# Kernel optimization log

Hardware: AMD Instinct MI355X
Metric: run time of the kernel (lower is better)

Reference implementation:

```python
import jax, jax.numpy as jnp
import numpy as np

B, N, C = 4, 2048, 768
H = 12
D = C // H  # head_dim = 64


def setup_inputs() -> dict:
    key = jax.random.key(0)
    k1, k2, k3, k4, k5 = jax.random.split(key, 5)
    s = 0.02
    return {
        "x": jax.random.normal(k1, (B, N, C), dtype=jnp.float32),
        "qkv_w": jax.random.normal(k2, (3 * C, C), dtype=jnp.float32) * s,
        "qkv_b": jax.random.normal(k3, (3 * C,), dtype=jnp.float32) * s,
        "proj_w": jax.random.normal(k4, (C, C), dtype=jnp.float32) * s,
        "proj_b": jax.random.normal(k5, (C,), dtype=jnp.float32) * s,
    }


def reference(x, qkv_w, qkv_b, proj_w, proj_b):
    b, n, c = x.shape
    # qkv projection (torch Linear: x @ W.T + b) -> [B,N,3,H,D] -> [3,B,H,N,D]
    qkv = (x @ qkv_w.T + qkv_b).reshape(b, n, 3, H, D).transpose(2, 0, 3, 1, 4)
    q, k, v = qkv[0], qkv[1], qkv[2]
    scale = D ** (-0.5)
    attn = jnp.einsum("bhqd,bhkd->bhqk", q, k) * scale
    attn = jax.nn.softmax(attn, axis=-1)
    # dropout is identity in eval mode
    out = jnp.einsum("bhqk,bhkd->bhqd", attn, v)  # [B,H,N,D]
    out = out.transpose(0, 2, 1, 3).reshape(b, n, c)
    return out @ proj_w.T + proj_b
```

## Files before the change

### kernel.cpp

```cpp
#include <hip/hip_runtime.h>
#include <hip/hip_bf16.h>
#include <stdint.h>

typedef __bf16 bf16_t;
typedef __bf16 bf16x8 __attribute__((ext_vector_type(8)));
typedef float f32x4 __attribute__((ext_vector_type(4)));
typedef unsigned int u32x4 __attribute__((ext_vector_type(4)));

#define NB 4
#define NH 12
#define ND 64
#define NN 2048
#define NC 768

__device__ __forceinline__ void async_copy16(const bf16_t* g, bf16_t* l) {
    __builtin_amdgcn_global_load_lds((__attribute__((address_space(1))) void*)(void*)g,
                                     (__attribute__((address_space(3))) void*)l, 16, 0, 0);
}

__device__ __forceinline__ unsigned pack_bf2(float a, float b) {
    union { bf16_t e[2]; unsigned u; } t;
    t.e[0] = (bf16_t)a;
    t.e[1] = (bf16_t)b;
    return t.u;
}

__global__ void cast_kernel(const float* __restrict__ src, bf16_t* __restrict__ dst, int n4) {
    int i = blockIdx.x * blockDim.x + threadIdx.x;
    if (i >= n4) return;
    float4 v = ((const float4*)src)[i];
    union { bf16_t e[4]; uint2 u; } t;
    t.e[0] = (bf16_t)v.x; t.e[1] = (bf16_t)v.y; t.e[2] = (bf16_t)v.z; t.e[3] = (bf16_t)v.w;
    ((uint2*)dst)[i] = t.u;
}

__device__ __forceinline__ int vperm(int s) {
    return (s & 32) | (((s >> 2) & 3) << 3) | (((s >> 4) & 1) << 2) | (s & 3);
}


template <bool ISV>
__launch_bounds__(256)
__global__ void qkv_gemm_kernel(const bf16_t* __restrict__ X, const bf16_t* __restrict__ W,
                                const float* __restrict__ bias,
                                bf16_t* __restrict__ Q, bf16_t* __restrict__ K, bf16_t* __restrict__ V,
                                int n0base)
{
    __shared__ __align__(16) bf16_t sA[128 * 64];
    __shared__ __align__(16) bf16_t sB[128 * 64];
    const int tid  = threadIdx.x;
    const int lane = tid & 63;
    const int w    = tid >> 6;
    const int wm   = w & 1, wn = w >> 1;
    const int m0   = blockIdx.x * 128;
    const int n0   = n0base + blockIdx.y * 128;
    const int lrow = lane & 15;
    const int quad = lane >> 4;
    const int arow = lane >> 3;
    const int gch  = (lane & 7) ^ arow;

    const int colbase = n0 + wn * 64;

    f32x4 zero = {0.f, 0.f, 0.f, 0.f};
    f32x4 acc[4][4];
#pragma unroll
    for (int i = 0; i < 4; ++i)
#pragma unroll
        for (int j = 0; j < 4; ++j) acc[i][j] = zero;

    for (int kt = 0; kt < NC; kt += 64) {
        __syncthreads();
        for (int c = w; c < 16; c += 4) {
            async_copy16(X + (size_t)(m0 + c * 8 + arow) * NC + kt + gch * 8, sA + c * 512);
            async_copy16(W + (size_t)(n0 + c * 8 + arow) * NC + kt + gch * 8, sB + c * 512);
        }
        __syncthreads();
#pragma unroll
        for (int hh = 0; hh < 2; ++hh) {
            bf16x8 xf[4], wf[4];
#pragma unroll
            for (int i = 0; i < 4; ++i) {
                int r = wm * 64 + i * 16 + lrow;
                xf[i] = *(const bf16x8*)(sA + r * 64 + (((hh * 4 + quad) ^ (r & 7)) * 8));
            }
#pragma unroll
            for (int j = 0; j < 4; ++j) {
                int r = wn * 64 + j * 16 + lrow;
                wf[j] = *(const bf16x8*)(sB + r * 64 + (((hh * 4 + quad) ^ (r & 7)) * 8));
            }
#pragma unroll
            for (int i = 0; i < 4; ++i)
#pragma unroll
                for (int j = 0; j < 4; ++j) {
                    if (ISV)
                        acc[i][j] = __builtin_amdgcn_mfma_f32_16x16x32_bf16(xf[i], wf[j], acc[i][j], 0, 0, 0);
                    else
                        acc[i][j] = __builtin_amdgcn_mfma_f32_16x16x32_bf16(wf[j], xf[i], acc[i][j], 0, 0, 0);
                }
        }
    }

    const float qscale = 0.125f * 1.44269504088896340736f;

    if (!ISV) {
        const int t3 = colbase / NC;
        const int h  = (colbase % NC) / ND;
        bf16_t* outb = t3 ? K : Q;
#pragma unroll
        for (int j = 0; j < 4; ++j) {
            const int dcol = j * 16 + quad * 4;
            const float4 bv4 = *(const float4*)(bias + colbase + dcol);
#pragma unroll
            for (int i = 0; i < 4; ++i) {
                const int tok = m0 + wm * 64 + i * 16 + lrow;
                const int bb = tok >> 11;
                const int nn = tok & 2047;
                union { bf16_t e[4]; uint2 u; } pk;
#pragma unroll
                for (int p = 0; p < 4; ++p) {
                    float val = acc[i][j][p] + (&bv4.x)[p];
                    if (t3 == 0) val *= qscale;
                    pk.e[p] = (bf16_t)val;
                }
                *(uint2*)(outb + ((size_t)(bb * NH + h) * NN + nn) * ND + dcol) = pk.u;
            }
        }
    } else {
        const int h = (colbase - 2 * NC) / ND;
#pragma unroll
        for (int j = 0; j < 4; ++j) {
            const int d  = j * 16 + lrow;
            const float bv = bias[colbase + d];
#pragma unroll
            for (int i = 0; i < 4; ++i) {
                const int tok0 = m0 + wm * 64 + i * 16 + quad * 4;
                const int bb = tok0 >> 11;
                const int nn = tok0 & 2047;
                union { bf16_t e[4]; uint2 u; } pk;
#pragma unroll
                for (int p = 0; p < 4; ++p) pk.e[p] = (bf16_t)(acc[i][j][p] + bv);
                const int pos = (nn & ~63) | vperm(nn & 63);
                *(uint2*)(V + ((size_t)(bb * NH + h) * ND + d) * NN + pos) = pk.u;
            }
        }
    }
}

__launch_bounds__(256, 4)
__global__ void attn_kernel(const bf16_t* __restrict__ Q, const bf16_t* __restrict__ K,
                            const bf16_t* __restrict__ Vt, bf16_t* __restrict__ O)
{
    __shared__ __align__(16) bf16_t sKV[4][64 * 64];
    bf16_t* sQ = sKV[0];
    const int tid  = threadIdx.x;
    const int lane = tid & 63;
    const int w    = tid >> 6;
    const int qt   = blockIdx.x;
    const int h    = blockIdx.y;
    const int b    = blockIdx.z;
    const int lrow = lane & 15;
    const int quad = lane >> 4;
    const int arow = lane >> 3;
    const int gch  = (lane & 7) ^ arow;
    const size_t head_off = (size_t)(b * NH + h) * NN * ND;
    const bf16_t* qh = Q  + head_off;
    const bf16_t* kh = K  + head_off;
    const bf16_t* vh = Vt + head_off;

#pragma unroll
    for (int c = 0; c < 4; ++c)
        async_copy16(qh + (size_t)(qt * 128 + (w * 4 + c) * 8 + arow) * ND + gch * 8,
                     sQ + (w * 4 + c) * 512);
    __syncthreads();

    bf16x8 qb[2][2];
#pragma unroll
    for (int qi = 0; qi < 2; ++qi)
#pragma unroll
        for (int hh = 0; hh < 2; ++hh) {
            int r = w * 32 + qi * 16 + lrow;
            qb[qi][hh] = *(const bf16x8*)(sQ + r * 64 + (((hh * 4 + quad) ^ (r & 7)) * 8));
        }

    int off[4][2];
#pragma unroll
    for (int blk = 0; blk < 4; ++blk) {
        int r = blk * 16 + lrow;
        off[blk][0] = r * 64 + ((quad ^ (r & 7)) * 8);
        off[blk][1] = r * 64 + (((4 + quad) ^ (r & 7)) * 8);
    }

    f32x4 zero = {0.f, 0.f, 0.f, 0.f};
    f32x4 o[2][4];
#pragma unroll
    for (int qi = 0; qi < 2; ++qi)
#pragma unroll
        for (int db = 0; db < 4; ++db) o[qi][db] = zero;
    float l_i[2] = {0.f, 0.f};

    const bf16_t* kp = kh + (size_t)(w * 16 + arow) * ND + gch * 8;
    const bf16_t* vp = vh + (size_t)(w * 16 + arow) * NN + gch * 8;

    for (int it = 0; it < NN / 128; ++it) {
        __syncthreads();
        async_copy16(kp,               sKV[0] + w * 1024);
        async_copy16(kp + 8 * ND,      sKV[0] + w * 1024 + 512);
        async_copy16(kp + 64 * ND,     sKV[1] + w * 1024);
        async_copy16(kp + 72 * ND,     sKV[1] + w * 1024 + 512);
        async_copy16(vp,               sKV[2] + w * 1024);
        async_copy16(vp + 8 * NN,      sKV[2] + w * 1024 + 512);
        async_copy16(vp + 64,          sKV[3] + w * 1024);
        async_copy16(vp + 8 * NN + 64, sKV[3] + w * 1024 + 512);
        __syncthreads();
        kp += 128 * ND;
        vp += 128;

#pragma unroll
        for (int half = 0; half < 2; ++half) {
            const bf16_t* sKh = sKV[half];
            const bf16_t* sVh = sKV[2 + half];

            f32x4 s[2][4];
#pragma unroll
            for (int blk = 0; blk < 4; ++blk) {
                bf16x8 a0 = *(const bf16x8*)(sKh + off[blk][0]);
                bf16x8 a1 = *(const bf16x8*)(sKh + off[blk][1]);
#pragma unroll
                for (int qi = 0; qi < 2; ++qi) {
                    f32x4 z = zero;
                    z = __builtin_amdgcn_mfma_f32_16x16x32_bf16(a0, qb[qi][0], z, 0, 0, 0);
                    z = __builtin_amdgcn_mfma_f32_16x16x32_bf16(a1, qb[qi][1], z, 0, 0, 0);
                    s[qi][blk] = z;
                }
            }

            bf16x8 pe[2][2];
#pragma unroll
            for (int qi = 0; qi < 2; ++qi) {
                u32x4 pu0 = {0, 0, 0, 0}, pu1 = {0, 0, 0, 0};
                float r0 = 0.f, r1 = 0.f;
#pragma unroll
                for (int blk = 0; blk < 4; ++blk) {
                    float e0 = __builtin_amdgcn_exp2f(s[qi][blk][0]);
                    float e1 = __builtin_amdgcn_exp2f(s[qi][blk][1]);
                    float e2 = __builtin_amdgcn_exp2f(s[qi][blk][2]);
                    float e3 = __builtin_amdgcn_exp2f(s[qi][blk][3]);
                    r0 += e0 + e1;
                    r1 += e2 + e3;
                    unsigned lo = pack_bf2(e0, e1), hi = pack_bf2(e2, e3);
                    if (blk == 0)      { pu0[0] = lo; pu0[1] = hi; }
                    else if (blk == 1) { pu0[2] = lo; pu0[3] = hi; }
                    else if (blk == 2) { pu1[0] = lo; pu1[1] = hi; }
                    else               { pu1[2] = lo; pu1[3] = hi; }
                }
                pe[qi][0] = __builtin_bit_cast(bf16x8, pu0);
                pe[qi][1] = __builtin_bit_cast(bf16x8, pu1);
                l_i[qi] += r0 + r1;
            }

#pragma unroll
            for (int db = 0; db < 4; ++db) {
                bf16x8 v0 = *(const bf16x8*)(sVh + off[db][0]);
                bf16x8 v1 = *(const bf16x8*)(sVh + off[db][1]);
#pragma unroll
                for (int qi = 0; qi < 2; ++qi) {
                    o[qi][db] = __builtin_amdgcn_mfma_f32_16x16x32_bf16(v0, pe[qi][0], o[qi][db], 0, 0, 0);
                    o[qi][db] = __builtin_amdgcn_mfma_f32_16x16x32_bf16(v1, pe[qi][1], o[qi][db], 0, 0, 0);
                }
            }
        }
    }

#pragma unroll
    for (int qi = 0; qi < 2; ++qi) {
        float l = l_i[qi];
        l += __shfl_xor(l, 16);
        l += __shfl_xor(l, 32);
        const float rl = 1.0f / l;
        const int n = qt * 128 + w * 32 + qi * 16 + lrow;
        const size_t rowoff = ((size_t)(b * NN + n)) * NC + h * ND;
#pragma unroll
        for (int db = 0; db < 4; ++db) {
            union { bf16_t e[4]; uint2 u; } pk;
#pragma unroll
            for (int p = 0; p < 4; ++p) pk.e[p] = (bf16_t)(o[qi][db][p] * rl);
            *(uint2*)(O + rowoff + db * 16 + quad * 4) = pk.u;
        }
    }
}

__launch_bounds__(256)
__global__ void proj_gemm_kernel(const bf16_t* __restrict__ A, const bf16_t* __restrict__ W,
                                 const float* __restrict__ bias, float* __restrict__ out)
{
    __shared__ __align__(16) bf16_t sA[128 * 64];
    __shared__ __align__(16) bf16_t sB[128 * 64];
    const int tid  = threadIdx.x;
    const int lane = tid & 63;
    const int w    = tid >> 6;
    const int wm   = w & 1, wn = w >> 1;
    const int m0   = blockIdx.x * 128;
    const int n0   = blockIdx.y * 128;
    const int lrow = lane & 15;
    const int quad = lane >> 4;
    const int arow = lane >> 3;
    const int gch  = (lane & 7) ^ arow;

    f32x4 zero = {0.f, 0.f, 0.f, 0.f};
    f32x4 acc[4][4];
#pragma unroll
    for (int i = 0; i < 4; ++i)
#pragma unroll
        for (int j = 0; j < 4; ++j) acc[i][j] = zero;

    for (int kt = 0; kt < NC; kt += 64) {
        __syncthreads();
        for (int c = w; c < 16; c += 4) {
            async_copy16(A + (size_t)(m0 + c * 8 + arow) * NC + kt + gch * 8, sA + c * 512);
            async_copy16(W + (size_t)(n0 + c * 8 + arow) * NC + kt + gch * 8, sB + c * 512);
        }
        __syncthreads();
#pragma unroll
        for (int hh = 0; hh < 2; ++hh) {
            bf16x8 xf[4], wf[4];
#pragma unroll
            for (int i = 0; i < 4; ++i) {
                int r = wm * 64 + i * 16 + lrow;
                xf[i] = *(const bf16x8*)(sA + r * 64 + (((hh * 4 + quad) ^ (r & 7)) * 8));
            }
#pragma unroll
            for (int j = 0; j < 4; ++j) {
                int r = wn * 64 + j * 16 + lrow;
                wf[j] = *(const bf16x8*)(sB + r * 64 + (((hh * 4 + quad) ^ (r & 7)) * 8));
            }
#pragma unroll
            for (int i = 0; i < 4; ++i)
#pragma unroll
                for (int j = 0; j < 4; ++j)
                    acc[i][j] = __builtin_amdgcn_mfma_f32_16x16x32_bf16(wf[j], xf[i], acc[i][j], 0, 0, 0);
        }
    }

#pragma unroll
    for (int j = 0; j < 4; ++j) {
        const int colg0 = n0 + wn * 64 + j * 16 + quad * 4;
        const float4 bv4 = *(const float4*)(bias + colg0);
#pragma unroll
        for (int i = 0; i < 4; ++i) {
            const int tok = m0 + wm * 64 + i * 16 + lrow;
            float4 val;
#pragma unroll
            for (int p = 0; p < 4; ++p) (&val.x)[p] = acc[i][j][p] + (&bv4.x)[p];
            *(float4*)(out + (size_t)tok * NC + colg0) = val;
        }
    }
}

extern "C" void kernel_launch(void* const* d_in, const int* in_sizes, int n_in,
                              void* d_out, int out_size, void* d_ws, size_t ws_size,
                              hipStream_t stream) {
    const float* x      = (const float*)d_in[0];
    const float* qkv_w  = (const float*)d_in[1];
    const float* qkv_b  = (const float*)d_in[2];
    const float* proj_w = (const float*)d_in[3];
    const float* proj_b = (const float*)d_in[4];
    float* out = (float*)d_out;

    char* ws = (char*)d_ws;
    bf16_t* xb    = (bf16_t*)ws; ws += (size_t)8192 * 768 * 2;
    bf16_t* wqkv  = (bf16_t*)ws; ws += (size_t)2304 * 768 * 2;
    bf16_t* wproj = (bf16_t*)ws; ws += (size_t)768 * 768 * 2;
    bf16_t* qb    = (bf16_t*)ws; ws += (size_t)NB * NH * NN * ND * 2;
    bf16_t* kb    = (bf16_t*)ws; ws += (size_t)NB * NH * NN * ND * 2;
    bf16_t* vb    = (bf16_t*)ws; ws += (size_t)NB * NH * NN * ND * 2;
    bf16_t* ab    = (bf16_t*)ws; ws += (size_t)8192 * 768 * 2;

    cast_kernel<<<(8192 * 768 / 4 + 255) / 256, 256, 0, stream>>>(x, xb, 8192 * 768 / 4);
    cast_kernel<<<(2304 * 768 / 4 + 255) / 256, 256, 0, stream>>>(qkv_w, wqkv, 2304 * 768 / 4);
    cast_kernel<<<(768 * 768 / 4 + 255) / 256, 256, 0, stream>>>(proj_w, wproj, 768 * 768 / 4);

    qkv_gemm_kernel<false><<<dim3(8192 / 128, 12), 256, 0, stream>>>(xb, wqkv, qkv_b, qb, kb, vb, 0);
    qkv_gemm_kernel<true><<<dim3(8192 / 128, 6), 256, 0, stream>>>(xb, wqkv, qkv_b, qb, kb, vb, 1536);
    attn_kernel<<<dim3(NN / 128, NH, NB), 256, 0, stream>>>(qb, kb, vb, ab);
    proj_gemm_kernel<<<dim3(8192 / 128, 768 / 128), 256, 0, stream>>>(ab, wproj, proj_b, out);
}
```

Before: 238.7 us.

## Fuse casts and QKV launches, double-buffer attention KV tiles, MFMA row sums

Merges the three cast launches into one kernel and the two QKV GEMM launches into a single grid with a unified MFMA operand order. The attention loop moves from 128-key tiles with two barriers to 64-key double-buffered K/V tiles that prefetch the next tile while computing the current one. Softmax row sums are now taken with an MFMA against a ones vector instead of scalar adds and shuffles. The epilogues now emit scalar bf16/fp32 stores for Q, K and the projection output instead of vector stores, which may cost write coalescing.

```diff
diff --git a/kernel.cpp b/kernel.cpp
--- a/kernel.cpp
+++ b/kernel.cpp
@@ -25,13 +25,21 @@
     return t.u;
 }
 
-__global__ void cast_kernel(const float* __restrict__ src, bf16_t* __restrict__ dst, int n4) {
+__global__ void cast3_kernel(const float* __restrict__ s0, bf16_t* __restrict__ d0, int n0,
+                             const float* __restrict__ s1, bf16_t* __restrict__ d1, int n1,
+                             const float* __restrict__ s2, bf16_t* __restrict__ d2, int n2) {
     int i = blockIdx.x * blockDim.x + threadIdx.x;
-    if (i >= n4) return;
-    float4 v = ((const float4*)src)[i];
+    const float* s;
+    bf16_t* d;
+    int j;
+    if (i < n0)           { s = s0; d = d0; j = i; }
+    else if (i < n0 + n1) { s = s1; d = d1; j = i - n0; }
+    else if (i < n0 + n1 + n2) { s = s2; d = d2; j = i - n0 - n1; }
+    else return;
+    float4 v = ((const float4*)s)[j];
     union { bf16_t e[4]; uint2 u; } t;
     t.e[0] = (bf16_t)v.x; t.e[1] = (bf16_t)v.y; t.e[2] = (bf16_t)v.z; t.e[3] = (bf16_t)v.w;
-    ((uint2*)dst)[i] = t.u;
+    ((uint2*)d)[j] = t.u;
 }
 
 __device__ __forceinline__ int vperm(int s) {
@@ -39,12 +47,10 @@
 }
 
 
-template <bool ISV>
 __launch_bounds__(256)
 __global__ void qkv_gemm_kernel(const bf16_t* __restrict__ X, const bf16_t* __restrict__ W,
                                 const float* __restrict__ bias,
-                                bf16_t* __restrict__ Q, bf16_t* __restrict__ K, bf16_t* __restrict__ V,
-                                int n0base)
+                                bf16_t* __restrict__ Q, bf16_t* __restrict__ K, bf16_t* __restrict__ V)
 {
     __shared__ __align__(16) bf16_t sA[128 * 64];
     __shared__ __align__(16) bf16_t sB[128 * 64];
@@ -53,14 +59,12 @@
     const int w    = tid >> 6;
     const int wm   = w & 1, wn = w >> 1;
     const int m0   = blockIdx.x * 128;
-    const int n0   = n0base + blockIdx.y * 128;
+    const int n0   = blockIdx.y * 128;
     const int lrow = lane & 15;
     const int quad = lane >> 4;
     const int arow = lane >> 3;
     const int gch  = (lane & 7) ^ arow;
 
-    const int colbase = n0 + wn * 64;
-
     f32x4 zero = {0.f, 0.f, 0.f, 0.f};
     f32x4 acc[4][4];
 #pragma unroll
@@ -77,70 +81,53 @@
         __syncthreads();
 #pragma unroll
         for (int hh = 0; hh < 2; ++hh) {
-            bf16x8 xf[4], wf[4];
+            bf16x8 af[4], bfr[4];
 #pragma unroll
             for (int i = 0; i < 4; ++i) {
                 int r = wm * 64 + i * 16 + lrow;
-                xf[i] = *(const bf16x8*)(sA + r * 64 + (((hh * 4 + quad) ^ (r & 7)) * 8));
+                af[i] = *(const bf16x8*)(sA + r * 64 + (((hh * 4 + quad) ^ (r & 7)) * 8));
             }
 #pragma unroll
             for (int j = 0; j < 4; ++j) {
                 int r = wn * 64 + j * 16 + lrow;
-                wf[j] = *(const bf16x8*)(sB + r * 64 + (((hh * 4 + quad) ^ (r & 7)) * 8));
+                bfr[j] = *(const bf16x8*)(sB + r * 64 + (((hh * 4 + quad) ^ (r & 7)) * 8));
             }
 #pragma unroll
             for (int i = 0; i < 4; ++i)
 #pragma unroll
-                for (int j = 0; j < 4; ++j) {
-                    if (ISV)
-                        acc[i][j] = __builtin_amdgcn_mfma_f32_16x16x32_bf16(xf[i], wf[j], acc[i][j], 0, 0, 0);
-                    else
-                        acc[i][j] = __builtin_amdgcn_mfma_f32_16x16x32_bf16(wf[j], xf[i], acc[i][j], 0, 0, 0);
-                }
-        }
-    }
-
+                for (int j = 0; j < 4; ++j)
+                    acc[i][j] = __builtin_amdgcn_mfma_f32_16x16x32_bf16(af[i], bfr[j], acc[i][j], 0, 0, 0);
+        }
+    }
+
+    const int colbase = n0 + wn * 64;
+    const int t3 = colbase / NC;
+    const int h  = (colbase % NC) / ND;
     const float qscale = 0.125f * 1.44269504088896340736f;
 
-    if (!ISV) {
-        const int t3 = colbase / NC;
-        const int h  = (colbase % NC) / ND;
-        bf16_t* outb = t3 ? K : Q;
-#pragma unroll
-        for (int j = 0; j < 4; ++j) {
-            const int dcol = j * 16 + quad * 4;
-            const float4 bv4 = *(const float4*)(bias + colbase + dcol);
-#pragma unroll
-            for (int i = 0; i < 4; ++i) {
-                const int tok = m0 + wm * 64 + i * 16 + lrow;
-                const int bb = tok >> 11;
-                const int nn = tok & 2047;
-                union { bf16_t e[4]; uint2 u; } pk;
-#pragma unroll
-                for (int p = 0; p < 4; ++p) {
-                    float val = acc[i][j][p] + (&bv4.x)[p];
-                    if (t3 == 0) val *= qscale;
-                    pk.e[p] = (bf16_t)val;
-                }
-                *(uint2*)(outb + ((size_t)(bb * NH + h) * NN + nn) * ND + dcol) = pk.u;
-            }
-        }
-    } else {
-        const int h = (colbase - 2 * NC) / ND;
-#pragma unroll
-        for (int j = 0; j < 4; ++j) {
-            const int d  = j * 16 + lrow;
-            const float bv = bias[colbase + d];
-#pragma unroll
-            for (int i = 0; i < 4; ++i) {
-                const int tok0 = m0 + wm * 64 + i * 16 + quad * 4;
-                const int bb = tok0 >> 11;
-                const int nn = tok0 & 2047;
+#pragma unroll
+    for (int j = 0; j < 4; ++j) {
+        const int d  = j * 16 + lrow;
+        const float bv = bias[colbase + d];
+#pragma unroll
+        for (int i = 0; i < 4; ++i) {
+            const int rowg = m0 + wm * 64 + i * 16 + quad * 4;
+            const int bb = rowg >> 11;
+            const int nn = rowg & 2047;
+            if (t3 == 2) {
                 union { bf16_t e[4]; uint2 u; } pk;
 #pragma unroll
                 for (int p = 0; p < 4; ++p) pk.e[p] = (bf16_t)(acc[i][j][p] + bv);
                 const int pos = (nn & ~63) | vperm(nn & 63);
                 *(uint2*)(V + ((size_t)(bb * NH + h) * ND + d) * NN + pos) = pk.u;
+            } else {
+                bf16_t* outb = t3 ? K : Q;
+#pragma unroll
+                for (int p = 0; p < 4; ++p) {
+                    float val = acc[i][j][p] + bv;
+                    if (t3 == 0) val *= qscale;
+                    outb[((size_t)(bb * NH + h) * NN + nn + p) * ND + d] = (bf16_t)val;
+                }
             }
         }
     }
@@ -150,8 +137,9 @@
 __global__ void attn_kernel(const bf16_t* __restrict__ Q, const bf16_t* __restrict__ K,
                             const bf16_t* __restrict__ Vt, bf16_t* __restrict__ O)
 {
-    __shared__ __align__(16) bf16_t sKV[4][64 * 64];
-    bf16_t* sQ = sKV[0];
+    __shared__ __align__(16) bf16_t sK[2][64 * 64];
+    __shared__ __align__(16) bf16_t sV[2][64 * 64];
+    bf16_t* sQ = sK[0];
     const int tid  = threadIdx.x;
     const int lane = tid & 63;
     const int w    = tid >> 6;
@@ -181,6 +169,11 @@
             int r = w * 32 + qi * 16 + lrow;
             qb[qi][hh] = *(const bf16x8*)(sQ + r * 64 + (((hh * 4 + quad) ^ (r & 7)) * 8));
         }
+    __syncthreads();
+
+    bf16x8 ones;
+#pragma unroll
+    for (int p = 0; p < 8; ++p) ones[p] = (bf16_t)1.0f;
 
     int off[4][2];
 #pragma unroll
@@ -196,87 +189,85 @@
     for (int qi = 0; qi < 2; ++qi)
 #pragma unroll
         for (int db = 0; db < 4; ++db) o[qi][db] = zero;
-    float l_i[2] = {0.f, 0.f};
+    f32x4 lacc[2] = {zero, zero};
 
     const bf16_t* kp = kh + (size_t)(w * 16 + arow) * ND + gch * 8;
     const bf16_t* vp = vh + (size_t)(w * 16 + arow) * NN + gch * 8;
 
-    for (int it = 0; it < NN / 128; ++it) {
-        __syncthreads();
-        async_copy16(kp,               sKV[0] + w * 1024);
-        async_copy16(kp + 8 * ND,      sKV[0] + w * 1024 + 512);
-        async_copy16(kp + 64 * ND,     sKV[1] + w * 1024);
-        async_copy16(kp + 72 * ND,     sKV[1] + w * 1024 + 512);
-        async_copy16(vp,               sKV[2] + w * 1024);
-        async_copy16(vp + 8 * NN,      sKV[2] + w * 1024 + 512);
-        async_copy16(vp + 64,          sKV[3] + w * 1024);
-        async_copy16(vp + 8 * NN + 64, sKV[3] + w * 1024 + 512);
-        __syncthreads();
-        kp += 128 * ND;
-        vp += 128;
-
-#pragma unroll
-        for (int half = 0; half < 2; ++half) {
-            const bf16_t* sKh = sKV[half];
-            const bf16_t* sVh = sKV[2 + half];
-
-            f32x4 s[2][4];
+    async_copy16(kp,          sK[0] + w * 1024);
+    async_copy16(kp + 8 * ND, sK[0] + w * 1024 + 512);
+    async_copy16(vp,          sV[0] + w * 1024);
+    async_copy16(vp + 8 * NN, sV[0] + w * 1024 + 512);
+    kp += 64 * ND; vp += 64;
+    __syncthreads();
+
+    int cur = 0;
+    for (int it = 0; it < NN / 64; ++it) {
+        if (it + 1 < NN / 64) {
+            bf16_t* dK = sK[cur ^ 1] + w * 1024;
+            bf16_t* dV = sV[cur ^ 1] + w * 1024;
+            async_copy16(kp,          dK);
+            async_copy16(kp + 8 * ND, dK + 512);
+            async_copy16(vp,          dV);
+            async_copy16(vp + 8 * NN, dV + 512);
+            kp += 64 * ND; vp += 64;
+        }
+        const bf16_t* sKh = sK[cur];
+        const bf16_t* sVh = sV[cur];
+
+        f32x4 s[2][4];
+#pragma unroll
+        for (int blk = 0; blk < 4; ++blk) {
+            bf16x8 a0 = *(const bf16x8*)(sKh + off[blk][0]);
+            bf16x8 a1 = *(const bf16x8*)(sKh + off[blk][1]);
+#pragma unroll
+            for (int qi = 0; qi < 2; ++qi) {
+                f32x4 z = zero;
+                z = __builtin_amdgcn_mfma_f32_16x16x32_bf16(a0, qb[qi][0], z, 0, 0, 0);
+                z = __builtin_amdgcn_mfma_f32_16x16x32_bf16(a1, qb[qi][1], z, 0, 0, 0);
+                s[qi][blk] = z;
+            }
+        }
+
+        bf16x8 pe[2][2];
+#pragma unroll
+        for (int qi = 0; qi < 2; ++qi) {
+            u32x4 pu0 = {0, 0, 0, 0}, pu1 = {0, 0, 0, 0};
 #pragma unroll
             for (int blk = 0; blk < 4; ++blk) {
-                bf16x8 a0 = *(const bf16x8*)(sKh + off[blk][0]);
-                bf16x8 a1 = *(const bf16x8*)(sKh + off[blk][1]);
-#pragma unroll
-                for (int qi = 0; qi < 2; ++qi) {
-                    f32x4 z = zero;
-                    z = __builtin_amdgcn_mfma_f32_16x16x32_bf16(a0, qb[qi][0], z, 0, 0, 0);
-                    z = __builtin_amdgcn_mfma_f32_16x16x32_bf16(a1, qb[qi][1], z, 0, 0, 0);
-                    s[qi][blk] = z;
-                }
-            }
-
-            bf16x8 pe[2][2];
+                float e0 = __builtin_amdgcn_exp2f(s[qi][blk][0]);
+                float e1 = __builtin_amdgcn_exp2f(s[qi][blk][1]);
+                float e2 = __builtin_amdgcn_exp2f(s[qi][blk][2]);
+                float e3 = __builtin_amdgcn_exp2f(s[qi][blk][3]);
+                unsigned lo = pack_bf2(e0, e1), hi = pack_bf2(e2, e3);
+                if (blk == 0)      { pu0[0] = lo; pu0[1] = hi; }
+                else if (blk == 1) { pu0[2] = lo; pu0[3] = hi; }
+                else if (blk == 2) { pu1[0] = lo; pu1[1] = hi; }
+                else               { pu1[2] = lo; pu1[3] = hi; }
+            }
+            pe[qi][0] = __builtin_bit_cast(bf16x8, pu0);
+            pe[qi][1] = __builtin_bit_cast(bf16x8, pu1);
+            lacc[qi] = __builtin_amdgcn_mfma_f32_16x16x32_bf16(ones, pe[qi][0], lacc[qi], 0, 0, 0);
+            lacc[qi] = __builtin_amdgcn_mfma_f32_16x16x32_bf16(ones, pe[qi][1], lacc[qi], 0, 0, 0);
+        }
+
+#pragma unroll
+        for (int db = 0; db < 4; ++db) {
+            bf16x8 v0 = *(const bf16x8*)(sVh + off[db][0]);
+            bf16x8 v1 = *(const bf16x8*)(sVh + off[db][1]);
 #pragma unroll
             for (int qi = 0; qi < 2; ++qi) {
-                u32x4 pu0 = {0, 0, 0, 0}, pu1 = {0, 0, 0, 0};
-                float r0 = 0.f, r1 = 0.f;
-#pragma unroll
-                for (int blk = 0; blk < 4; ++blk) {
-                    float e0 = __builtin_amdgcn_exp2f(s[qi][blk][0]);
-                    float e1 = __builtin_amdgcn_exp2f(s[qi][blk][1]);
-                    float e2 = __builtin_amdgcn_exp2f(s[qi][blk][2]);
-                    float e3 = __builtin_amdgcn_exp2f(s[qi][blk][3]);
-                    r0 += e0 + e1;
-                    r1 += e2 + e3;
-                    unsigned lo = pack_bf2(e0, e1), hi = pack_bf2(e2, e3);
-                    if (blk == 0)      { pu0[0] = lo; pu0[1] = hi; }
-                    else if (blk == 1) { pu0[2] = lo; pu0[3] = hi; }
-                    else if (blk == 2) { pu1[0] = lo; pu1[1] = hi; }
-                    else               { pu1[2] = lo; pu1[3] = hi; }
-                }
-                pe[qi][0] = __builtin_bit_cast(bf16x8, pu0);
-                pe[qi][1] = __builtin_bit_cast(bf16x8, pu1);
-                l_i[qi] += r0 + r1;
-            }
-
-#pragma unroll
-            for (int db = 0; db < 4; ++db) {
-                bf16x8 v0 = *(const bf16x8*)(sVh + off[db][0]);
-                bf16x8 v1 = *(const bf16x8*)(sVh + off[db][1]);
-#pragma unroll
-                for (int qi = 0; qi < 2; ++qi) {
-                    o[qi][db] = __builtin_amdgcn_mfma_f32_16x16x32_bf16(v0, pe[qi][0], o[qi][db], 0, 0, 0);
-                    o[qi][db] = __builtin_amdgcn_mfma_f32_16x16x32_bf16(v1, pe[qi][1], o[qi][db], 0, 0, 0);
-                }
-            }
-        }
+                o[qi][db] = __builtin_amdgcn_mfma_f32_16x16x32_bf16(v0, pe[qi][0], o[qi][db], 0, 0, 0);
+                o[qi][db] = __builtin_amdgcn_mfma_f32_16x16x32_bf16(v1, pe[qi][1], o[qi][db], 0, 0, 0);
+            }
+        }
+        __syncthreads();
+        cur ^= 1;
     }
 
 #pragma unroll
     for (int qi = 0; qi < 2; ++qi) {
-        float l = l_i[qi];
-        l += __shfl_xor(l, 16);
-        l += __shfl_xor(l, 32);
-        const float rl = 1.0f / l;
+        const float rl = 1.0f / lacc[qi][0];
         const int n = qt * 128 + w * 32 + qi * 16 + lrow;
         const size_t rowoff = ((size_t)(b * NN + n)) * NC + h * ND;
 #pragma unroll
@@ -322,36 +313,35 @@
         __syncthreads();
 #pragma unroll
         for (int hh = 0; hh < 2; ++hh) {
-            bf16x8 xf[4], wf[4];
+            bf16x8 af[4], bfr[4];
 #pragma unroll
             for (int i = 0; i < 4; ++i) {
                 int r = wm * 64 + i * 16 + lrow;
-                xf[i] = *(const bf16x8*)(sA + r * 64 + (((hh * 4 + quad) ^ (r & 7)) * 8));
+                af[i] = *(const bf16x8*)(sA + r * 64 + (((hh * 4 + quad) ^ (r & 7)) * 8));
             }
 #pragma unroll
             for (int j = 0; j < 4; ++j) {
                 int r = wn * 64 + j * 16 + lrow;
-                wf[j] = *(const bf16x8*)(sB + r * 64 + (((hh * 4 + quad) ^ (r & 7)) * 8));
+                bfr[j] = *(const bf16x8*)(sB + r * 64 + (((hh * 4 + quad) ^ (r & 7)) * 8));
             }
 #pragma unroll
             for (int i = 0; i < 4; ++i)
 #pragma unroll
                 for (int j = 0; j < 4; ++j)
-                    acc[i][j] = __builtin_amdgcn_mfma_f32_16x16x32_bf16(wf[j], xf[i], acc[i][j], 0, 0, 0);
+                    acc[i][j] = __builtin_amdgcn_mfma_f32_16x16x32_bf16(af[i], bfr[j], acc[i][j], 0, 0, 0);
         }
     }
 
 #pragma unroll
     for (int j = 0; j < 4; ++j) {
-        const int colg0 = n0 + wn * 64 + j * 16 + quad * 4;
-        const float4 bv4 = *(const float4*)(bias + colg0);
+        const int colg = n0 + wn * 64 + j * 16 + lrow;
+        const float bv = bias[colg];
 #pragma unroll
         for (int i = 0; i < 4; ++i) {
-            const int tok = m0 + wm * 64 + i * 16 + lrow;
-            float4 val;
-#pragma unroll
-            for (int p = 0; p < 4; ++p) (&val.x)[p] = acc[i][j][p] + (&bv4.x)[p];
-            *(float4*)(out + (size_t)tok * NC + colg0) = val;
+            const int rowg = m0 + wm * 64 + i * 16 + quad * 4;
+#pragma unroll
+            for (int p = 0; p < 4; ++p)
+                out[(size_t)(rowg + p) * NC + colg] = acc[i][j][p] + bv;
         }
     }
 }
@@ -375,12 +365,10 @@
     bf16_t* vb    = (bf16_t*)ws; ws += (size_t)NB * NH * NN * ND * 2;
     bf16_t* ab    = (bf16_t*)ws; ws += (size_t)8192 * 768 * 2;
 
-    cast_kernel<<<(8192 * 768 / 4 + 255) / 256, 256, 0, stream>>>(x, xb, 8192 * 768 / 4);
-    cast_kernel<<<(2304 * 768 / 4 + 255) / 256, 256, 0, stream>>>(qkv_w, wqkv, 2304 * 768 / 4);
-    cast_kernel<<<(768 * 768 / 4 + 255) / 256, 256, 0, stream>>>(proj_w, wproj, 768 * 768 / 4);
-
-    qkv_gemm_kernel<false><<<dim3(8192 / 128, 12), 256, 0, stream>>>(xb, wqkv, qkv_b, qb, kb, vb, 0);
-    qkv_gemm_kernel<true><<<dim3(8192 / 128, 6), 256, 0, stream>>>(xb, wqkv, qkv_b, qb, kb, vb, 1536);
+    const int c0 = 8192 * 768 / 4, c1 = 2304 * 768 / 4, c2 = 768 * 768 / 4;
+    cast3_kernel<<<(c0 + c1 + c2 + 255) / 256, 256, 0, stream>>>(x, xb, c0, qkv_w, wqkv, c1, proj_w, wproj, c2);
+
+    qkv_gemm_kernel<<<dim3(8192 / 128, 2304 / 128), 256, 0, stream>>>(xb, wqkv, qkv_b, qb, kb, vb);
     attn_kernel<<<dim3(NN / 128, NH, NB), 256, 0, stream>>>(qb, kb, vb, ab);
     proj_gemm_kernel<<<dim3(8192 / 128, 768 / 128), 256, 0, stream>>>(ab, wproj, proj_b, out);
 }
```

Result: faster. 212.6 us (-10.9%).
